# Optimization experiments

Measured on AMD Instinct MI355X. Metric: run time of the kernel, lower is better.

Reference implementation:

```python
import jax, jax.numpy as jnp
import numpy as np

D_MODEL = 512
D_FF = 4 * D_MODEL
NUM_EXPERTS = 8
TOP_K = 2
NUM_TASKS = 16
D_TASK = 64
BATCH = 8
SEQ = 4096
LN_EPS = 1e-5


def setup_inputs() -> dict:
    key = jax.random.key(0)
    ks = jax.random.split(key, 10)
    s_in = 1.0 / np.sqrt(D_MODEL)
    s_ff = 1.0 / np.sqrt(D_FF)
    s_g = 1.0 / np.sqrt(D_MODEL + D_TASK)
    return {
        "x": jax.random.normal(ks[0], (BATCH, SEQ, D_MODEL), jnp.float32),
        "task_id": jax.random.randint(ks[1], (BATCH,), 0, NUM_TASKS),
        "w1": jax.random.normal(ks[2], (NUM_EXPERTS, D_MODEL, D_FF), jnp.float32) * s_in,
        "b1": jnp.zeros((NUM_EXPERTS, D_FF), jnp.float32),
        "w2": jax.random.normal(ks[3], (NUM_EXPERTS, D_FF, D_MODEL), jnp.float32) * s_ff,
        "b2": jnp.zeros((NUM_EXPERTS, D_MODEL), jnp.float32),
        "task_emb": jax.random.normal(ks[4], (NUM_TASKS, D_TASK), jnp.float32),
        "gate_w": jax.random.normal(ks[5], (D_MODEL + D_TASK, NUM_EXPERTS), jnp.float32) * s_g,
        "gate_b": jnp.zeros((NUM_EXPERTS,), jnp.float32),
    }


def reference(x, task_id, w1, b1, w2, b2, task_emb, gate_w, gate_b):
    B, S, D = x.shape
    E = w1.shape[0]

    # F.layer_norm(x, x.shape[1:]): normalize over (seq, d_model) jointly, no affine
    mean = jnp.mean(x, axis=(1, 2), keepdims=True)
    var = jnp.var(x, axis=(1, 2), keepdims=True)
    x_norm = (x - mean) * jax.lax.rsqrt(var + LN_EPS)

    t_emb = task_emb[task_id]                       # [B, d_task]
    t_emb = jnp.broadcast_to(t_emb[:, None, :], (B, S, t_emb.shape[-1]))
    gate_in = jnp.concatenate([x_norm, t_emb], axis=-1)
    logits = gate_in @ gate_w + gate_b              # [B, S, E]

    topk_logits, topk_idx = jax.lax.top_k(logits, TOP_K)   # [B, S, K]
    topk_probs = jax.nn.softmax(topk_logits, axis=-1)

    flat_x = x.reshape(-1, D)                       # [T, D]
    flat_idx = topk_idx.reshape(-1, TOP_K)          # [T, K]
    flat_p = topk_probs.reshape(-1, TOP_K)          # [T, K]

    assign = jax.nn.one_hot(flat_idx, E, dtype=x.dtype)    # [T, K, E]
    combine = jnp.einsum("tk,tke->te", flat_p, assign)     # [T, E] per-token expert weight

    out = jnp.zeros_like(flat_x)
    for e in range(E):  # fixed small expert loop
        h = jax.nn.silu(flat_x @ w1[e] + b1[e])
        y = h @ w2[e] + b2[e]
        out = out + y * combine[:, e:e + 1]
    final_output = out.reshape(B, S, D)

    usage = jnp.sum(assign, axis=(0, 1))            # [E] assignment counts
    usage_mean = jnp.mean(usage) + 1e-6
    usage_std = jnp.std(usage, ddof=1)              # torch.std is unbiased
    lb_loss = (usage_std / usage_mean) ** 2

    return final_output, lb_loss, topk_idx, task_id
```

## Files before the change

kernel.cpp:

```cpp
#include <hip/hip_runtime.h>

#define NB      8
#define SEQ     4096
#define DM      512
#define DFF     2048
#define NE      8
#define NTOK    32768
#define NPB     2097152
#define MAXROWS 66560
#define MAXTILES 520

#define OUT_LB   16777216
#define OUT_TOPK 16777217
#define OUT_TASK 16842753

#define WS_BSTATS   0
#define WS_DMEAN    8192
#define WS_DRSTD    8256
#define WS_DCOLSUM  8320
#define WS_DTASK    8384
#define WS_HIST     8896
#define WS_CURSOR   8928
#define WS_SEGOFF   8960
#define WS_HDR_END  9216
#define WS_ROUTE_E  9216
#define WS_ROUTE_P  271360
#define WS_ATOK     533504
#define WS_APROB    799744
#define WS_TOKPOS   1065984
#define WS_RAW      1328128
#define WS_W1T      3425280
#define WS_W2T      20202496
#define WS_XB       36979712
#define WS_Y        70534144
#define WS_H        138691584

typedef __attribute__((ext_vector_type(4))) float  f32x4;
typedef __attribute__((ext_vector_type(8))) __bf16 bf16x8;
typedef __attribute__((ext_vector_type(8))) short  s16x8;

__device__ __forceinline__ unsigned short f2bf(float f) {
    unsigned int u = __builtin_bit_cast(unsigned int, f);
    u += 0x7FFFu + ((u >> 16) & 1u);
    return (unsigned short)(u >> 16);
}
__device__ __forceinline__ float bf2f(unsigned short b) {
    unsigned int u = ((unsigned int)b) << 16;
    return __builtin_bit_cast(float, u);
}
__device__ __forceinline__ unsigned int pkbf(float a, float b) {
    unsigned int r;
    asm("v_cvt_pk_bf16_f32 %0, %1, %2" : "=v"(r) : "v"(a), "v"(b));
    return r;
}

#define GLDS16(g, l)                                                              \
    __builtin_amdgcn_global_load_lds(                                             \
        (const __attribute__((address_space(1))) unsigned int*)(const void*)(g),  \
        (__attribute__((address_space(3))) unsigned int*)(void*)(l), 16, 0, 0)

__global__ void k_transpose_bf16(const float* __restrict__ in,
                                 unsigned short* __restrict__ outT,
                                 int R, int C) {
    __shared__ float tile[32][33];
    int e = blockIdx.z;
    const float* src = in + (size_t)e * R * C;
    unsigned short* dst = outT + (size_t)e * R * C;
    int tx = threadIdx.x & 31, ty = threadIdx.x >> 5;
    int c0 = blockIdx.x * 32, r0 = blockIdx.y * 32;
#pragma unroll
    for (int i = 0; i < 4; i++) {
        int r = r0 + ty + i * 8;
        tile[ty + i * 8][tx] = src[(size_t)r * C + c0 + tx];
    }
    __syncthreads();
#pragma unroll
    for (int i = 0; i < 4; i++) {
        int rr = c0 + ty + i * 8;
        dst[(size_t)rr * R + r0 + tx] = f2bf(tile[tx][ty + i * 8]);
    }
}

#define GQPAD 1032
__global__ void __launch_bounds__(256) k_xgate(const float* __restrict__ x,
                                               const float* __restrict__ gw,
                                               unsigned short* __restrict__ xb,
                                               double* __restrict__ bstats,
                                               double* __restrict__ raw) {
    __shared__ float gws[4 * GQPAD];
    int t = threadIdx.x;
#pragma unroll
    for (int i = 0; i < 16; i++) {
        int idx = i * 256 + t;
        int row = idx >> 3, e = idx & 7;
        gws[(row >> 7) * GQPAD + (row & 127) * 8 + e] = gw[idx];
    }
    __syncthreads();

    int token = blockIdx.x * 64 + (t >> 2);
    int q = t & 3;
    const float4* xp = (const float4*)(x + (size_t)token * DM + q * 128);
    unsigned short* xbp = xb + (size_t)token * DM + q * 128;
    const float* gq = &gws[q * GQPAD];

    double acc[8] = {0, 0, 0, 0, 0, 0, 0, 0};
    double s = 0.0, ss = 0.0;
#pragma unroll 4
    for (int i = 0; i < 32; i += 2) {
        float4 v0 = xp[i];
        float4 v1 = xp[i + 1];
        {
            double dx = v0.x, dy = v0.y, dz = v0.z, dw = v0.w;
            const float* g = &gq[i * 32];
#pragma unroll
            for (int e = 0; e < 8; e++)
                acc[e] += dx * (double)g[e] + dy * (double)g[8 + e]
                        + dz * (double)g[16 + e] + dw * (double)g[24 + e];
            s  += dx + dy + dz + dw;
            ss += dx * dx + dy * dy + dz * dz + dw * dw;
        }
        {
            double dx = v1.x, dy = v1.y, dz = v1.z, dw = v1.w;
            const float* g = &gq[(i + 1) * 32];
#pragma unroll
            for (int e = 0; e < 8; e++)
                acc[e] += dx * (double)g[e] + dy * (double)g[8 + e]
                        + dz * (double)g[16 + e] + dw * (double)g[24 + e];
            s  += dx + dy + dz + dw;
            ss += dx * dx + dy * dy + dz * dz + dw * dw;
        }
        s16x8 o = {(short)f2bf(v0.x), (short)f2bf(v0.y), (short)f2bf(v0.z), (short)f2bf(v0.w),
                   (short)f2bf(v1.x), (short)f2bf(v1.y), (short)f2bf(v1.z), (short)f2bf(v1.w)};
        *(s16x8*)(xbp + i * 4) = o;
    }

#pragma unroll
    for (int e = 0; e < 8; e++) {
        acc[e] += __shfl_xor(acc[e], 1);
        acc[e] += __shfl_xor(acc[e], 2);
    }
    if (q == 0) {
#pragma unroll
        for (int e = 0; e < 8; e++) raw[(size_t)token * 8 + e] = acc[e];
    }

    for (int o = 32; o; o >>= 1) { s += __shfl_down(s, o); ss += __shfl_down(ss, o); }
    __shared__ double as_[4], ass_[4];
    int w = t >> 6;
    if ((t & 63) == 0) { as_[w] = s; ass_[w] = ss; }
    __syncthreads();
    if (t == 0) {
        s  = as_[0] + as_[1] + as_[2] + as_[3];
        ss = ass_[0] + ass_[1] + ass_[2] + ass_[3];
        bstats[blockIdx.x * 2]     = s;
        bstats[blockIdx.x * 2 + 1] = ss;
    }
}

__global__ void k_finalize(const double* __restrict__ bstats,
                           double* __restrict__ dmean, double* __restrict__ drstd,
                           double* __restrict__ dcolsum, double* __restrict__ dtask,
                           const float* __restrict__ gw, const float* __restrict__ gb,
                           const float* __restrict__ temb, const int* __restrict__ task_id,
                           float* __restrict__ out_task) {
    int t = threadIdx.x;
    if (t < 8) {
        double s = 0.0, ss = 0.0;
        for (int i = 0; i < 64; i++) {
            s  += bstats[(t * 64 + i) * 2];
            ss += bstats[(t * 64 + i) * 2 + 1];
        }
        double N = (double)NPB;
        double m = s / N;
        double var = ss / N - m * m;
        dmean[t] = m;
        drstd[t] = 1.0 / sqrt(var + 1e-5);
    }
    __shared__ double colp[32][8];
    {
        int e = t & 7, g = t >> 3;
        double a = 0.0;
        for (int r = g * 16; r < g * 16 + 16; r++) a += (double)gw[r * 8 + e];
        colp[g][e] = a;
    }
    __syncthreads();
    if (t < 8) {
        double a = 0.0;
        for (int g = 0; g < 32; g++) a += colp[g][t];
        dcolsum[t] = a;
    }
    if (t < 64) {
        int b2 = t >> 3, e = t & 7;
        int tid = task_id[b2];
        double a = (double)gb[e];
        for (int d = 0; d < 64; d++)
            a += (double)temb[tid * 64 + d] * (double)gw[(512 + d) * 8 + e];
        dtask[t] = a;
    }
    if (t < 8) out_task[t] = (float)task_id[t];
}

__global__ void __launch_bounds__(256) k_topk(const double* __restrict__ raw,
                                              const double* __restrict__ dmean,
                                              const double* __restrict__ drstd,
                                              const double* __restrict__ dcolsum,
                                              const double* __restrict__ dtask,
                                              int* __restrict__ hist,
                                              int2* __restrict__ route_e,
                                              float2* __restrict__ route_p,
                                              float* __restrict__ out_topk) {
    __shared__ int lh[8];
    int t = threadIdx.x;
    if (t < 8) lh[t] = 0;
    __syncthreads();
    int token = blockIdx.x * 256 + t;
    int b = token >> 12;
    double m = dmean[b], rs = drstd[b];
    double lg[8];
#pragma unroll
    for (int e = 0; e < 8; e++)
        lg[e] = rs * (raw[(size_t)token * 8 + e] - m * dcolsum[e]) + dtask[b * 8 + e];
    int i0 = 0;
#pragma unroll
    for (int e = 1; e < 8; e++) if (lg[e] > lg[i0]) i0 = e;
    int i1 = (i0 == 0) ? 1 : 0;
#pragma unroll
    for (int e = 0; e < 8; e++) if (e != i0 && lg[e] > lg[i1]) i1 = e;
    double d = exp(lg[i1] - lg[i0]);
    double p0 = 1.0 / (1.0 + d);
    double p1 = d / (1.0 + d);
    out_topk[token * 2]     = (float)i0;
    out_topk[token * 2 + 1] = (float)i1;
    atomicAdd(&lh[i0], 1);
    atomicAdd(&lh[i1], 1);
    route_e[token] = make_int2(i0, i1);
    route_p[token] = make_float2((float)p0, (float)p1);
    __syncthreads();
    if (t < 8) atomicAdd(&hist[t], lh[t]);
}

__global__ void k_offsets_lb(const int* __restrict__ hist, int* __restrict__ seg_off,
                             float* __restrict__ out_lb) {
    if (threadIdx.x == 0) {
        int off = 0;
        double ssd = 0.0;
        for (int e = 0; e < 8; e++) {
            seg_off[e] = off;
            off += (hist[e] + 127) & ~127;
            double d = (double)hist[e] - 8192.0;
            ssd += d * d;
        }
        seg_off[8] = off;
        double stdv = sqrt(ssd / 7.0);
        double m = 8192.0 + 1e-6;
        double r = stdv / m;
        *out_lb = (float)(r * r);
    }
}

__global__ void __launch_bounds__(256) k_scatter(const int2* __restrict__ route_e,
                                                 const float2* __restrict__ route_p,
                                                 const int* __restrict__ seg_off,
                                                 int* __restrict__ cursor,
                                                 int* __restrict__ atok,
                                                 float* __restrict__ aprob,
                                                 int* __restrict__ tokpos) {
    __shared__ int lcount[8];
    __shared__ int lbase[8];
    int t = threadIdx.x;
    if (t < 8) lcount[t] = 0;
    __syncthreads();
    int tok = blockIdx.x * 256 + t;
    int2 e = route_e[tok];
    float2 p = route_p[tok];
    int p0 = atomicAdd(&lcount[e.x], 1);
    int p1 = atomicAdd(&lcount[e.y], 1);
    __syncthreads();
    if (t < 8) lbase[t] = atomicAdd(&cursor[t], lcount[t]);
    __syncthreads();
    int a0 = seg_off[e.x] + lbase[e.x] + p0;
    atok[a0] = tok; aprob[a0] = p.x;
    int a1 = seg_off[e.y] + lbase[e.y] + p1;
    atok[a1] = tok; aprob[a1] = p.y;
    tokpos[tok * 2]     = a0;
    tokpos[tok * 2 + 1] = a1;
}


__global__ void __launch_bounds__(256) k_gemm1(const unsigned short* __restrict__ xb,
                                               const unsigned short* __restrict__ w1t,
                                               const float* __restrict__ b1,
                                               const int* __restrict__ atok,
                                               const int* __restrict__ seg_off,
                                               unsigned short* __restrict__ H,
                                               int t0) {
    int nwg = (int)gridDim.x;
    int bid = (int)blockIdx.x;
    int wg = (bid & 7) * (nwg >> 3) + (bid >> 3);
    int xt = wg >> 4, y = wg & 15;
    int r0 = (t0 + xt) * 128;
    if (r0 >= seg_off[8]) return;
    int e = 0;
    while (seg_off[e + 1] <= r0) e++;
    int f0 = y * 128;

    int tid = threadIdx.x;
    int w = tid >> 6, l = tid & 63;
    int c = l & 7;

    __shared__ __align__(16) unsigned short As[2][128 * 64];
    __shared__ __align__(16) unsigned short Bs[2][128 * 64];

    const unsigned short* asrc[4];
    const unsigned short* bsrc[4];
    unsigned short*       adst[4];
    unsigned short*       bdst[4];
#pragma unroll
    for (int j = 0; j < 4; j++) {
        int R = w * 32 + j * 8 + (l >> 3);
        int cs = c ^ (R & 7);
        int tok = atok[r0 + R]; if (tok < 0) tok = 0;
        asrc[j] = xb + (size_t)tok * DM + cs * 8;
        bsrc[j] = w1t + ((size_t)e * DFF + f0 + R) * DM + cs * 8;
        adst[j] = &As[0][(size_t)(w * 32 + j * 8) * 64];
        bdst[j] = &Bs[0][(size_t)(w * 32 + j * 8) * 64];
    }

    f32x4 acc[4][4] = {};
    int wr = w >> 1, wc = w & 1, lr = l & 15, q = l >> 4;

#pragma unroll
    for (int j = 0; j < 4; j++) { GLDS16(asrc[j], adst[j]); GLDS16(bsrc[j], bdst[j]); }

    int cur = 0;
    for (int it = 0; it < DM / 64; ++it) {
        if (it + 1 < DM / 64) {
            int kn = (it + 1) * 64;
            int off = (cur ^ 1) * 128 * 64;
#pragma unroll
            for (int j = 0; j < 4; j++) {
                GLDS16(asrc[j] + kn, adst[j] + off);
                GLDS16(bsrc[j] + kn, bdst[j] + off);
            }
            asm volatile("s_waitcnt vmcnt(8)" ::: "memory");
        } else {
            asm volatile("s_waitcnt vmcnt(0)" ::: "memory");
        }
        __builtin_amdgcn_s_barrier();
        __builtin_amdgcn_sched_barrier(0);
        __builtin_amdgcn_s_setprio(1);
        const unsigned short* Ab = &As[cur][0];
        const unsigned short* Bb = &Bs[cur][0];
#pragma unroll
        for (int h = 0; h < 2; h++) {
            bf16x8 af[4], bfv[4];
#pragma unroll
            for (int m = 0; m < 4; m++) {
                int R = wr * 64 + m * 16 + lr;
                af[m] = *(const bf16x8*)&Ab[R * 64 + (((h << 2) + q) ^ (R & 7)) * 8];
            }
#pragma unroll
            for (int n = 0; n < 4; n++) {
                int R = wc * 64 + n * 16 + lr;
                bfv[n] = *(const bf16x8*)&Bb[R * 64 + (((h << 2) + q) ^ (R & 7)) * 8];
            }
#pragma unroll
            for (int m = 0; m < 4; m++)
#pragma unroll
                for (int n = 0; n < 4; n++)
                    acc[m][n] = __builtin_amdgcn_mfma_f32_16x16x32_bf16(bfv[n], af[m], acc[m][n], 0, 0, 0);
        }
        __builtin_amdgcn_s_setprio(0);
        __builtin_amdgcn_sched_barrier(0);
        asm volatile("" ::: "memory");
        __builtin_amdgcn_s_barrier();
        cur ^= 1;
    }

    const float* b1e = b1 + e * DFF + f0;
#pragma unroll
    for (int m = 0; m < 4; m++) {
        int r = wr * 64 + m * 16 + lr;
        unsigned short* hrow = H + ((size_t)xt * 128 + r) * DFF + f0;
#pragma unroll
        for (int n = 0; n < 4; n++) {
            int fc = wc * 64 + n * 16 + q * 4;
            float4 bias = *(const float4*)(b1e + fc);
            float v0 = acc[m][n][0] + bias.x; v0 = v0 / (1.0f + __expf(-v0));
            float v1 = acc[m][n][1] + bias.y; v1 = v1 / (1.0f + __expf(-v1));
            float v2 = acc[m][n][2] + bias.z; v2 = v2 / (1.0f + __expf(-v2));
            float v3 = acc[m][n][3] + bias.w; v3 = v3 / (1.0f + __expf(-v3));
            *(uint2*)(hrow + fc) = make_uint2(pkbf(v0, v1), pkbf(v2, v3));
        }
    }
}

__global__ void __launch_bounds__(256) k_gemm2(const unsigned short* __restrict__ H,
                                               const unsigned short* __restrict__ w2t,
                                               const int* __restrict__ seg_off,
                                               unsigned short* __restrict__ Y,
                                               int t0) {
    int nwg = (int)gridDim.x;
    int bid = (int)blockIdx.x;
    int wg = (bid & 7) * (nwg >> 3) + (bid >> 3);
    int xt = wg >> 2, y = wg & 3;
    int r0 = (t0 + xt) * 128;
    if (r0 >= seg_off[8]) return;
    int e = 0;
    while (seg_off[e + 1] <= r0) e++;
    int d0 = y * 128;

    int tid = threadIdx.x;
    int w = tid >> 6, l = tid & 63;
    int c = l & 7;

    __shared__ __align__(16) unsigned short As[2][128 * 64];
    __shared__ __align__(16) unsigned short Bs[2][128 * 64];

    const unsigned short* asrc[4];
    const unsigned short* bsrc[4];
    unsigned short*       adst[4];
    unsigned short*       bdst[4];
#pragma unroll
    for (int j = 0; j < 4; j++) {
        int R = w * 32 + j * 8 + (l >> 3);
        int cs = c ^ (R & 7);
        asrc[j] = H + ((size_t)xt * 128 + R) * DFF + cs * 8;
        bsrc[j] = w2t + ((size_t)e * DM + d0 + R) * DFF + cs * 8;
        adst[j] = &As[0][(size_t)(w * 32 + j * 8) * 64];
        bdst[j] = &Bs[0][(size_t)(w * 32 + j * 8) * 64];
    }

    f32x4 acc[4][4] = {};
    int wr = w >> 1, wc = w & 1, lr = l & 15, q = l >> 4;

#pragma unroll
    for (int j = 0; j < 4; j++) { GLDS16(asrc[j], adst[j]); GLDS16(bsrc[j], bdst[j]); }

    int cur = 0;
    for (int it = 0; it < DFF / 64; ++it) {
        if (it + 1 < DFF / 64) {
            int kn = (it + 1) * 64;
            int off = (cur ^ 1) * 128 * 64;
#pragma unroll
            for (int j = 0; j < 4; j++) {
                GLDS16(asrc[j] + kn, adst[j] + off);
                GLDS16(bsrc[j] + kn, bdst[j] + off);
            }
            asm volatile("s_waitcnt vmcnt(8)" ::: "memory");
        } else {
            asm volatile("s_waitcnt vmcnt(0)" ::: "memory");
        }
        __builtin_amdgcn_s_barrier();
        __builtin_amdgcn_sched_barrier(0);
        __builtin_amdgcn_s_setprio(1);
        const unsigned short* Ab = &As[cur][0];
        const unsigned short* Bb = &Bs[cur][0];
#pragma unroll
        for (int h = 0; h < 2; h++) {
            bf16x8 af[4], bfv[4];
#pragma unroll
            for (int m = 0; m < 4; m++) {
                int R = wr * 64 + m * 16 + lr;
                af[m] = *(const bf16x8*)&Ab[R * 64 + (((h << 2) + q) ^ (R & 7)) * 8];
            }
#pragma unroll
            for (int n = 0; n < 4; n++) {
                int R = wc * 64 + n * 16 + lr;
                bfv[n] = *(const bf16x8*)&Bb[R * 64 + (((h << 2) + q) ^ (R & 7)) * 8];
            }
#pragma unroll
            for (int m = 0; m < 4; m++)
#pragma unroll
                for (int n = 0; n < 4; n++)
                    acc[m][n] = __builtin_amdgcn_mfma_f32_16x16x32_bf16(bfv[n], af[m], acc[m][n], 0, 0, 0);
        }
        __builtin_amdgcn_s_setprio(0);
        __builtin_amdgcn_sched_barrier(0);
        asm volatile("" ::: "memory");
        __builtin_amdgcn_s_barrier();
        cur ^= 1;
    }

#pragma unroll
    for (int m = 0; m < 4; m++) {
        int r = wr * 64 + m * 16 + lr;
        unsigned short* yrow = Y + (size_t)(r0 + r) * DM + d0;
#pragma unroll
        for (int n = 0; n < 4; n++) {
            int dc = wc * 64 + n * 16 + q * 4;
            *(uint2*)(yrow + dc) = make_uint2(pkbf(acc[m][n][0], acc[m][n][1]),
                                              pkbf(acc[m][n][2], acc[m][n][3]));
        }
    }
}

__global__ void __launch_bounds__(256) k_combine(const unsigned short* __restrict__ Y,
                                                 const float* __restrict__ b2,
                                                 const int* __restrict__ tokpos,
                                                 const int2* __restrict__ route_e,
                                                 const float2* __restrict__ route_p,
                                                 float* __restrict__ out) {
    int gt = blockIdx.x * 256 + threadIdx.x;
    int token = gt >> 6;
    int cbase = (gt & 63) * 8;
    int2 e = route_e[token];
    float2 p = route_p[token];
    int a0 = tokpos[token * 2], a1 = tokpos[token * 2 + 1];
    s16x8 y0 = *(const s16x8*)(Y + (size_t)a0 * DM + cbase);
    s16x8 y1 = *(const s16x8*)(Y + (size_t)a1 * DM + cbase);
    const float4* bb0 = (const float4*)(b2 + e.x * DM + cbase);
    const float4* bb1 = (const float4*)(b2 + e.y * DM + cbase);
    float4 b00 = bb0[0], b01 = bb0[1];
    float4 b10 = bb1[0], b11 = bb1[1];
    float r[8];
    r[0] = p.x * (bf2f((unsigned short)y0[0]) + b00.x) + p.y * (bf2f((unsigned short)y1[0]) + b10.x);
    r[1] = p.x * (bf2f((unsigned short)y0[1]) + b00.y) + p.y * (bf2f((unsigned short)y1[1]) + b10.y);
    r[2] = p.x * (bf2f((unsigned short)y0[2]) + b00.z) + p.y * (bf2f((unsigned short)y1[2]) + b10.z);
    r[3] = p.x * (bf2f((unsigned short)y0[3]) + b00.w) + p.y * (bf2f((unsigned short)y1[3]) + b10.w);
    r[4] = p.x * (bf2f((unsigned short)y0[4]) + b01.x) + p.y * (bf2f((unsigned short)y1[4]) + b11.x);
    r[5] = p.x * (bf2f((unsigned short)y0[5]) + b01.y) + p.y * (bf2f((unsigned short)y1[5]) + b11.y);
    r[6] = p.x * (bf2f((unsigned short)y0[6]) + b01.z) + p.y * (bf2f((unsigned short)y1[6]) + b11.z);
    r[7] = p.x * (bf2f((unsigned short)y0[7]) + b01.w) + p.y * (bf2f((unsigned short)y1[7]) + b11.w);
    float* op = out + (size_t)token * DM + cbase;
    *(float4*)op       = make_float4(r[0], r[1], r[2], r[3]);
    *(float4*)(op + 4) = make_float4(r[4], r[5], r[6], r[7]);
}

extern "C" void kernel_launch(void* const* d_in, const int* in_sizes, int n_in,
                              void* d_out, int out_size, void* d_ws, size_t ws_size,
                              hipStream_t stream) {
    const float* x       = (const float*)d_in[0];
    const int*   task_id = (const int*)d_in[1];
    const float* w1      = (const float*)d_in[2];
    const float* b1      = (const float*)d_in[3];
    const float* w2      = (const float*)d_in[4];
    const float* b2      = (const float*)d_in[5];
    const float* temb    = (const float*)d_in[6];
    const float* gw      = (const float*)d_in[7];
    const float* gb      = (const float*)d_in[8];
    float* out = (float*)d_out;

    char* ws = (char*)d_ws;
    double* bstats   = (double*)(ws + WS_BSTATS);
    double* dmean    = (double*)(ws + WS_DMEAN);
    double* drstd    = (double*)(ws + WS_DRSTD);
    double* dcolsum  = (double*)(ws + WS_DCOLSUM);
    double* dtask    = (double*)(ws + WS_DTASK);
    int*    hist     = (int*)(ws + WS_HIST);
    int*    cursor   = (int*)(ws + WS_CURSOR);
    int*    seg_off  = (int*)(ws + WS_SEGOFF);
    int2*   route_e  = (int2*)(ws + WS_ROUTE_E);
    float2* route_p  = (float2*)(ws + WS_ROUTE_P);
    int*    atok     = (int*)(ws + WS_ATOK);
    float*  aprob    = (float*)(ws + WS_APROB);
    int*    tokpos   = (int*)(ws + WS_TOKPOS);
    double* raw      = (double*)(ws + WS_RAW);
    unsigned short* w1t = (unsigned short*)(ws + WS_W1T);
    unsigned short* w2t = (unsigned short*)(ws + WS_W2T);
    unsigned short* xb  = (unsigned short*)(ws + WS_XB);
    unsigned short* Y   = (unsigned short*)(ws + WS_Y);
    unsigned short* H   = (unsigned short*)(ws + WS_H);

    int TPC = (int)((ws_size - (size_t)WS_H) / (size_t)(128 * DFF * 2));
    if (TPC > 128) TPC = 128;
    TPC &= ~1;
    if (TPC < 2) TPC = 2;

    hipMemsetAsync(ws, 0, WS_HDR_END, stream);
    hipMemsetAsync(ws + WS_ATOK, 0xFF, (size_t)MAXROWS * sizeof(int), stream);

    k_transpose_bf16<<<dim3(DFF / 32, DM / 32, NE), 256, 0, stream>>>(w1, w1t, DM, DFF);
    k_transpose_bf16<<<dim3(DM / 32, DFF / 32, NE), 256, 0, stream>>>(w2, w2t, DFF, DM);

    k_xgate<<<NTOK / 64, 256, 0, stream>>>(x, gw, xb, bstats, raw);
    k_finalize<<<1, 256, 0, stream>>>(bstats, dmean, drstd, dcolsum, dtask,
                                      gw, gb, temb, task_id, out + OUT_TASK);
    k_topk<<<NTOK / 256, 256, 0, stream>>>(raw, dmean, drstd, dcolsum, dtask,
                                           hist, route_e, route_p, out + OUT_TOPK);
    k_offsets_lb<<<1, 64, 0, stream>>>(hist, seg_off, out + OUT_LB);
    k_scatter<<<NTOK / 256, 256, 0, stream>>>(route_e, route_p, seg_off, cursor,
                                              atok, aprob, tokpos);

    for (int t0 = 0; t0 < MAXTILES; t0 += TPC) {
        k_gemm1<<<TPC * 16, 256, 0, stream>>>(xb, w1t, b1, atok, seg_off, H, t0);
        k_gemm2<<<TPC * 4, 256, 0, stream>>>(H, w2t, seg_off, Y, t0);
    }
    k_combine<<<NTOK / 4, 256, 0, stream>>>(Y, b2, tokpos, route_e, route_p, out);
}
```

Before: 545.8 us.

## Make each gemm1 workgroup loop over four FF tiles, prefetching across tiles

Each gemm1 workgroup now computes four consecutive 128-wide FF column tiles for its 128-row token tile, instead of one. The loads for the next tile's first K-slice are issued during the last K iteration of the current tile, so the double-buffered pipeline continues across tiles. The grid shrinks by a factor of four. This cuts per-workgroup launch and setup overhead, including the seg_off scan and atok gather, and may let gathered x rows stay in cache between tiles. The costs are fewer workgroups per chunk, which lowers parallelism and may leave CUs idle, and a longer serial body per workgroup.

```diff
diff --git a/kernel.cpp b/kernel.cpp
--- a/kernel.cpp
+++ b/kernel.cpp
@@ -297,100 +297,123 @@
     int nwg = (int)gridDim.x;
     int bid = (int)blockIdx.x;
     int wg = (bid & 7) * (nwg >> 3) + (bid >> 3);
-    int xt = wg >> 4, y = wg & 15;
+    int xt = wg >> 2, fg = wg & 3;
     int r0 = (t0 + xt) * 128;
     if (r0 >= seg_off[8]) return;
     int e = 0;
     while (seg_off[e + 1] <= r0) e++;
-    int f0 = y * 128;
 
     int tid = threadIdx.x;
     int w = tid >> 6, l = tid & 63;
     int c = l & 7;
+    int wr = w >> 1, wc = w & 1, lr = l & 15, q = l >> 4;
 
     __shared__ __align__(16) unsigned short As[2][128 * 64];
     __shared__ __align__(16) unsigned short Bs[2][128 * 64];
 
     const unsigned short* asrc[4];
-    const unsigned short* bsrc[4];
     unsigned short*       adst[4];
     unsigned short*       bdst[4];
+    int Rr[4], csr[4];
 #pragma unroll
     for (int j = 0; j < 4; j++) {
         int R = w * 32 + j * 8 + (l >> 3);
         int cs = c ^ (R & 7);
+        Rr[j] = R; csr[j] = cs;
         int tok = atok[r0 + R]; if (tok < 0) tok = 0;
         asrc[j] = xb + (size_t)tok * DM + cs * 8;
-        bsrc[j] = w1t + ((size_t)e * DFF + f0 + R) * DM + cs * 8;
         adst[j] = &As[0][(size_t)(w * 32 + j * 8) * 64];
         bdst[j] = &Bs[0][(size_t)(w * 32 + j * 8) * 64];
     }
-
-    f32x4 acc[4][4] = {};
-    int wr = w >> 1, wc = w & 1, lr = l & 15, q = l >> 4;
-
-#pragma unroll
-    for (int j = 0; j < 4; j++) { GLDS16(asrc[j], adst[j]); GLDS16(bsrc[j], bdst[j]); }
-
-    int cur = 0;
-    for (int it = 0; it < DM / 64; ++it) {
-        if (it + 1 < DM / 64) {
-            int kn = (it + 1) * 64;
-            int off = (cur ^ 1) * 128 * 64;
-#pragma unroll
-            for (int j = 0; j < 4; j++) {
-                GLDS16(asrc[j] + kn, adst[j] + off);
-                GLDS16(bsrc[j] + kn, bdst[j] + off);
+    const size_t w1base = (size_t)e * DFF;
+
+    {
+        int f0 = (fg * 4) * 128;
+#pragma unroll
+        for (int j = 0; j < 4; j++) {
+            GLDS16(asrc[j], adst[j]);
+            GLDS16(w1t + (w1base + f0 + Rr[j]) * DM + csr[j] * 8, bdst[j]);
+        }
+    }
+
+    for (int ft = 0; ft < 4; ++ft) {
+        int f0 = (fg * 4 + ft) * 128;
+        const unsigned short* bsrc[4];
+#pragma unroll
+        for (int j = 0; j < 4; j++)
+            bsrc[j] = w1t + (w1base + f0 + Rr[j]) * DM + csr[j] * 8;
+
+        f32x4 acc[4][4] = {};
+        int cur = 0;
+#pragma unroll
+        for (int it = 0; it < 8; ++it) {
+            if (it < 7) {
+                int kn = (it + 1) * 64;
+                int off = (cur ^ 1) * 128 * 64;
+#pragma unroll
+                for (int j = 0; j < 4; j++) {
+                    GLDS16(asrc[j] + kn, adst[j] + off);
+                    GLDS16(bsrc[j] + kn, bdst[j] + off);
+                }
+                asm volatile("s_waitcnt vmcnt(8)" ::: "memory");
+            } else if (ft < 3) {
+                int f0n = (fg * 4 + ft + 1) * 128;
+                int off = (cur ^ 1) * 128 * 64;
+#pragma unroll
+                for (int j = 0; j < 4; j++) {
+                    GLDS16(asrc[j], adst[j] + off);
+                    GLDS16(w1t + (w1base + f0n + Rr[j]) * DM + csr[j] * 8, bdst[j] + off);
+                }
+                asm volatile("s_waitcnt vmcnt(8)" ::: "memory");
+            } else {
+                asm volatile("s_waitcnt vmcnt(0)" ::: "memory");
             }
-            asm volatile("s_waitcnt vmcnt(8)" ::: "memory");
-        } else {
-            asm volatile("s_waitcnt vmcnt(0)" ::: "memory");
-        }
-        __builtin_amdgcn_s_barrier();
-        __builtin_amdgcn_sched_barrier(0);
-        __builtin_amdgcn_s_setprio(1);
-        const unsigned short* Ab = &As[cur][0];
-        const unsigned short* Bb = &Bs[cur][0];
-#pragma unroll
-        for (int h = 0; h < 2; h++) {
-            bf16x8 af[4], bfv[4];
-#pragma unroll
-            for (int m = 0; m < 4; m++) {
-                int R = wr * 64 + m * 16 + lr;
-                af[m] = *(const bf16x8*)&Ab[R * 64 + (((h << 2) + q) ^ (R & 7)) * 8];
+            __builtin_amdgcn_s_barrier();
+            __builtin_amdgcn_sched_barrier(0);
+            __builtin_amdgcn_s_setprio(1);
+            const unsigned short* Ab = &As[cur][0];
+            const unsigned short* Bb = &Bs[cur][0];
+#pragma unroll
+            for (int h = 0; h < 2; h++) {
+                bf16x8 af[4], bfv[4];
+#pragma unroll
+                for (int m = 0; m < 4; m++) {
+                    int R = wr * 64 + m * 16 + lr;
+                    af[m] = *(const bf16x8*)&Ab[R * 64 + (((h << 2) + q) ^ (R & 7)) * 8];
+                }
+#pragma unroll
+                for (int n = 0; n < 4; n++) {
+                    int R = wc * 64 + n * 16 + lr;
+                    bfv[n] = *(const bf16x8*)&Bb[R * 64 + (((h << 2) + q) ^ (R & 7)) * 8];
+                }
+#pragma unroll
+                for (int m = 0; m < 4; m++)
+#pragma unroll
+                    for (int n = 0; n < 4; n++)
+                        acc[m][n] = __builtin_amdgcn_mfma_f32_16x16x32_bf16(bfv[n], af[m], acc[m][n], 0, 0, 0);
             }
+            __builtin_amdgcn_s_setprio(0);
+            __builtin_amdgcn_sched_barrier(0);
+            asm volatile("" ::: "memory");
+            __builtin_amdgcn_s_barrier();
+            cur ^= 1;
+        }
+
+        const float* b1e = b1 + e * DFF + f0;
+#pragma unroll
+        for (int m = 0; m < 4; m++) {
+            int r = wr * 64 + m * 16 + lr;
+            unsigned short* hrow = H + ((size_t)xt * 128 + r) * DFF + f0;
 #pragma unroll
             for (int n = 0; n < 4; n++) {
-                int R = wc * 64 + n * 16 + lr;
-                bfv[n] = *(const bf16x8*)&Bb[R * 64 + (((h << 2) + q) ^ (R & 7)) * 8];
+                int fc = wc * 64 + n * 16 + q * 4;
+                float4 bias = *(const float4*)(b1e + fc);
+                float v0 = acc[m][n][0] + bias.x; v0 = v0 / (1.0f + __expf(-v0));
+                float v1 = acc[m][n][1] + bias.y; v1 = v1 / (1.0f + __expf(-v1));
+                float v2 = acc[m][n][2] + bias.z; v2 = v2 / (1.0f + __expf(-v2));
+                float v3 = acc[m][n][3] + bias.w; v3 = v3 / (1.0f + __expf(-v3));
+                *(uint2*)(hrow + fc) = make_uint2(pkbf(v0, v1), pkbf(v2, v3));
             }
-#pragma unroll
-            for (int m = 0; m < 4; m++)
-#pragma unroll
-                for (int n = 0; n < 4; n++)
-                    acc[m][n] = __builtin_amdgcn_mfma_f32_16x16x32_bf16(bfv[n], af[m], acc[m][n], 0, 0, 0);
-        }
-        __builtin_amdgcn_s_setprio(0);
-        __builtin_amdgcn_sched_barrier(0);
-        asm volatile("" ::: "memory");
-        __builtin_amdgcn_s_barrier();
-        cur ^= 1;
-    }
-
-    const float* b1e = b1 + e * DFF + f0;
-#pragma unroll
-    for (int m = 0; m < 4; m++) {
-        int r = wr * 64 + m * 16 + lr;
-        unsigned short* hrow = H + ((size_t)xt * 128 + r) * DFF + f0;
-#pragma unroll
-        for (int n = 0; n < 4; n++) {
-            int fc = wc * 64 + n * 16 + q * 4;
-            float4 bias = *(const float4*)(b1e + fc);
-            float v0 = acc[m][n][0] + bias.x; v0 = v0 / (1.0f + __expf(-v0));
-            float v1 = acc[m][n][1] + bias.y; v1 = v1 / (1.0f + __expf(-v1));
-            float v2 = acc[m][n][2] + bias.z; v2 = v2 / (1.0f + __expf(-v2));
-            float v3 = acc[m][n][3] + bias.w; v3 = v3 / (1.0f + __expf(-v3));
-            *(uint2*)(hrow + fc) = make_uint2(pkbf(v0, v1), pkbf(v2, v3));
         }
     }
 }
@@ -583,7 +606,7 @@
                                               atok, aprob, tokpos);
 
     for (int t0 = 0; t0 < MAXTILES; t0 += TPC) {
-        k_gemm1<<<TPC * 16, 256, 0, stream>>>(xb, w1t, b1, atok, seg_off, H, t0);
+        k_gemm1<<<TPC * 4, 256, 0, stream>>>(xb, w1t, b1, atok, seg_off, H, t0);
         k_gemm2<<<TPC * 4, 256, 0, stream>>>(H, w2t, seg_off, Y, t0);
     }
     k_combine<<<NTOK / 4, 256, 0, stream>>>(Y, b2, tokpos, route_e, route_p, out);
```

New measurement: 678.3 us. 24.3% more time.
